# Performance work log

Hardware: AMD Instinct MI355X
Metric: run time of the kernel (lower is better)

The kernel has to match this reference:

```python
import jax, jax.numpy as jnp
import numpy as np
from jax import lax

T, B = 256, 4096
H = 64  # lstm hidden/input size


def setup_inputs() -> dict:
    key = jax.random.key(0)
    ks = jax.random.split(key, 20)
    s = 0.1
    return {
        "x": jax.random.normal(ks[0], (T * B, 9), jnp.float32),
        "done": jax.random.randint(ks[1], (T * B,), 0, 2).astype(jnp.int32),
        "h0": jax.random.normal(ks[2], (1, B, H), jnp.float32),
        "c0": jax.random.normal(ks[3], (1, B, H), jnp.float32),
        # root MLP: Linear(9,32) ReLU Linear(32,64) ReLU (stored [in,out])
        "Wr1": jax.random.normal(ks[4], (9, 32), jnp.float32) * s,
        "br1": jnp.zeros((32,), jnp.float32),
        "Wr2": jax.random.normal(ks[5], (32, H), jnp.float32) * s,
        "br2": jnp.zeros((H,), jnp.float32),
        # LSTM(64,64): gate order i,f,g,o; stored [in, 4H]
        "Wih": jax.random.normal(ks[6], (H, 4 * H), jnp.float32) * s,
        "Whh": jax.random.normal(ks[7], (H, 4 * H), jnp.float32) * s,
        "b_lstm": jnp.zeros((4 * H,), jnp.float32),  # bias_ih + bias_hh (both init 0)
        # critic: Linear(64,16) Tanh Linear(16,8) Tanh Linear(8,1)
        "Wc1": jax.random.normal(ks[8], (H, 16), jnp.float32) * s,
        "bc1": jnp.zeros((16,), jnp.float32),
        "Wc2": jax.random.normal(ks[9], (16, 8), jnp.float32) * s,
        "bc2": jnp.zeros((8,), jnp.float32),
        "Wc3": jax.random.normal(ks[10], (8, 1), jnp.float32) * s,
        "bc3": jnp.zeros((1,), jnp.float32),
    }


def reference(x, done, h0, c0, Wr1, br1, Wr2, br2, Wih, Whh, b_lstm,
              Wc1, bc1, Wc2, bc2, Wc3, bc3):
    b = h0.shape[1]
    # root MLP on all T*B rows at once
    hidden = jax.nn.relu(jax.nn.relu(x @ Wr1 + br1) @ Wr2 + br2)  # [T*B, 64]
    t = hidden.shape[0] // b
    hid = hidden.reshape(t, b, H)
    d = done.reshape(t, b).astype(hidden.dtype)
    # precompute input projection for all timesteps (hoisted out of the scan)
    xp = hid @ Wih + b_lstm  # [T, B, 4H]

    def step(carry, inp):
        h, c = carry
        xpt, dt = inp
        m = (1.0 - dt)[:, None]  # reset state where episode is done
        h = h * m
        c = c * m
        g = xpt + h @ Whh  # [B, 4H]
        gi, gf, gg, go = jnp.split(g, 4, axis=-1)
        c = jax.nn.sigmoid(gf) * c + jax.nn.sigmoid(gi) * jnp.tanh(gg)
        h = jax.nn.sigmoid(go) * jnp.tanh(c)
        return (h, c), h

    (_, _), hs = lax.scan(step, (h0[0], c0[0]), (xp, d))
    new_hidden = hs.reshape(t * b, H)  # flatten like torch.cat + flatten(0,1)
    # critic head (get_value)
    v = jnp.tanh(new_hidden @ Wc1 + bc1)
    v = jnp.tanh(v @ Wc2 + bc2)
    return v @ Wc3 + bc3  # [T*B, 1]
```

## Files before the change

### kernel.cpp

```cpp
#include <hip/hip_runtime.h>
#include <hip/hip_bf16.h>


#define TT 256
#define BB 4096
#define TBROWS (TT * BB)
#define LOG2E 1.44269504088896340736f

typedef short bf16x8 __attribute__((ext_vector_type(8)));
typedef float f32x4 __attribute__((ext_vector_type(4)));

__device__ __forceinline__ unsigned bfbits(float x) {
  unsigned u = __float_as_uint(x);
  return (u + 0x7fffu + ((u >> 16) & 1u)) >> 16;
}
__device__ __forceinline__ unsigned pkbf(float lo, float hi) {
  return bfbits(lo) | (bfbits(hi) << 16);
}
__device__ __forceinline__ unsigned short cvt1bf(float x) {
  unsigned pk;
  asm("v_cvt_pk_bf16_f32 %0, %1, %2" : "=v"(pk) : "v"(x), "v"(x));
  return (unsigned short)pk;
}
__device__ __forceinline__ float rcpf_(float x) { return __builtin_amdgcn_rcpf(x); }
__device__ __forceinline__ float exp2f_(float x) { return __builtin_amdgcn_exp2f(x); }

#define BAR_LDS()                                                   \
  do {                                                              \
    asm volatile("s_waitcnt lgkmcnt(0)" ::: "memory");              \
    __builtin_amdgcn_s_barrier();                                   \
    asm volatile("" ::: "memory");                                  \
  } while (0)

__global__ __launch_bounds__(256) void k1m(const float* __restrict__ x,
                                           const float* __restrict__ Wr1,
                                           const float* __restrict__ br1,
                                           const float* __restrict__ Wr2,
                                           const float* __restrict__ br2,
                                           unsigned short* __restrict__ hb) {
  __shared__ int sBr1[2 * 256];
  __shared__ int sBr2[4 * 256];
  __shared__ float sx[4][208];
  __shared__ int h1s[4][324];

  const int tid = threadIdx.x;
  const int lane = tid & 63, wid = tid >> 6;
  const int g4 = lane >> 4, l15 = lane & 15;

  for (int i = tid; i < 512; i += 256) {
    int nt = i >> 8, rem = i & 255;
    int L = rem >> 2, d = rem & 3;
    int u = nt * 16 + (L & 15);
    int k0 = (L >> 4) * 4 + d;
    float v0 = (k0 < 9) ? Wr1[k0 * 32 + u] : 0.f;
    sBr1[i] = (int)bfbits(v0);
  }
  for (int i = tid; i < 1024; i += 256) {
    int nt = i >> 8, rem = i & 255;
    int L = rem >> 2, d = rem & 3;
    int u = nt * 16 + (L & 15);
    int p = (L >> 4) * 4 + d;
    sBr2[i] = (int)pkbf(Wr2[p * 64 + u], Wr2[(p + 16) * 64 + u]);
  }
  __syncthreads();

  float br1v[2] = {br1[l15], br1[16 + l15]};
  float br2v[4];
#pragma unroll
  for (int nt = 0; nt < 4; ++nt) br2v[nt] = br2[nt * 16 + l15];

  long gw = (long)blockIdx.x * 4 + wid;
  long nw = (long)gridDim.x * 4;
  for (long row0 = gw * 16; row0 < TBROWS; row0 += nw * 16) {
    {
      int j = lane;
      float v = x[row0 * 9 + j];
      int r = (j * 456) >> 12; int cc = j - r * 9;
      sx[wid][r * 12 + cc] = v;
      j = lane + 64;
      v = x[row0 * 9 + j];
      r = (j * 456) >> 12; cc = j - r * 9;
      sx[wid][r * 12 + cc] = v;
      if (lane < 16) {
        j = lane + 128;
        v = x[row0 * 9 + j];
        r = (j * 456) >> 12; cc = j - r * 9;
        sx[wid][r * 12 + cc] = v;
      }
    }
    float4 xq = *(const float4*)&sx[wid][l15 * 12 + g4 * 4];
    union { unsigned u[4]; bf16x8 v; } A1;
#pragma unroll
    for (int d = 0; d < 4; ++d) {
      float v = ((const float*)&xq)[d];
      v = (g4 * 4 + d < 9) ? v : 0.f;
      A1.u[d] = bfbits(v);
    }
    f32x4 c1[2];
#pragma unroll
    for (int nt = 0; nt < 2; ++nt) {
      c1[nt] = (f32x4){br1v[nt], br1v[nt], br1v[nt], br1v[nt]};
      c1[nt] = __builtin_amdgcn_mfma_f32_16x16x32_bf16(
          A1.v, *(const bf16x8*)&sBr1[nt * 256 + lane * 4], c1[nt], 0, 0, 0);
    }
#pragma unroll
    for (int r = 0; r < 4; ++r)
      h1s[wid][(g4 * 4 + r) * 20 + l15] =
          (int)pkbf(fmaxf(c1[0][r], 0.f), fmaxf(c1[1][r], 0.f));
    bf16x8 A2 = *(const bf16x8*)&h1s[wid][l15 * 20 + g4 * 4];
    f32x4 c2[4];
#pragma unroll
    for (int nt = 0; nt < 4; ++nt) {
      c2[nt] = (f32x4){br2v[nt], br2v[nt], br2v[nt], br2v[nt]};
      c2[nt] = __builtin_amdgcn_mfma_f32_16x16x32_bf16(
          A2, *(const bf16x8*)&sBr2[nt * 256 + lane * 4], c2[nt], 0, 0, 0);
    }
#pragma unroll
    for (int nt = 0; nt < 4; ++nt)
#pragma unroll
      for (int r = 0; r < 4; ++r)
        hb[(row0 + g4 * 4 + r) * 64 + nt * 16 + l15] =
            (unsigned short)bfbits(fmaxf(c2[nt][r], 0.f));
  }
}

__global__ __launch_bounds__(320) void k2m(
    const unsigned short* __restrict__ hb, const int* __restrict__ done,
    const float* __restrict__ h0, const float* __restrict__ c0,
    const float* __restrict__ Wih, const float* __restrict__ Whh,
    const float* __restrict__ bl,
    const float* __restrict__ Wc1, const float* __restrict__ bc1,
    const float* __restrict__ Wc2, const float* __restrict__ bc2,
    const float* __restrict__ Wc3, const float* __restrict__ bc3,
    float* __restrict__ out) {
  __shared__ __align__(16) unsigned short hT2[2][16 * 72];
  __shared__ float sv1[16 * 20];
  __shared__ __align__(16) float smask[TT * 16];
  __shared__ int sdn[TT * 16];

  const int tid = threadIdx.x;
  const int lane = tid & 63;
  const int wid = tid >> 6;
  const int g4 = lane >> 4, l15 = lane & 15;
  const int base_b = blockIdx.x * 16;

  for (int i = tid; i < TT * 16; i += 320) {
    int d = done[(long)(i >> 4) * BB + base_b + (i & 15)];
    sdn[i] = d;
    smask[i] = 1.f - (float)d;
  }

  union frag { unsigned u[4]; bf16x8 v; };
  frag Bih[4][2], Bhh[4][2];
  frag Bc1[2];
  float wc2a[16], wc2b[16];
  float c[4];
  f32x4 bias_acc[4];
  float bc1s = 0.f, bc2s0 = 0.f, bc2s1 = 0.f, wc3a = 0.f, wc3b = 0.f, bc3r = 0.f;

  if (wid < 4) {
#pragma unroll
    for (int g = 0; g < 4; ++g) {
      int nt = g * 4 + wid;
      int col = nt * 16 + l15;
      float sc = (g == 2) ? 2.f * LOG2E : LOG2E;
#pragma unroll
      for (int q = 0; q < 2; ++q)
#pragma unroll
        for (int d = 0; d < 4; ++d) {
          int k0 = q * 32 + g4 * 8 + 2 * d;
          Bih[g][q].u[d] = pkbf(Wih[k0 * 256 + col] * sc, Wih[(k0 + 1) * 256 + col] * sc);
          Bhh[g][q].u[d] = pkbf(Whh[k0 * 256 + col] * sc, Whh[(k0 + 1) * 256 + col] * sc);
        }
      float bv = bl[nt * 16 + l15] * sc;
      bias_acc[g] = (f32x4){bv, bv, bv, bv};
    }
#pragma unroll
    for (int r = 0; r < 4; ++r) {
      int row = base_b + g4 * 4 + r;
      float m0 = 1.f - (float)done[row];
      c[r] = c0[row * 64 + wid * 16 + l15] * m0;
      hT2[1][(g4 * 4 + r) * 72 + wid * 16 + l15] =
          (unsigned short)bfbits(h0[row * 64 + wid * 16 + l15]);
    }
  } else {
    float S = 2.f * LOG2E;
#pragma unroll
    for (int q = 0; q < 2; ++q)
#pragma unroll
      for (int d = 0; d < 4; ++d) {
        int k0 = q * 32 + g4 * 8 + 2 * d;
        Bc1[q].u[d] = pkbf(Wc1[k0 * 16 + l15] * S, Wc1[(k0 + 1) * 16 + l15] * S);
      }
#pragma unroll
    for (int k = 0; k < 16; ++k) {
      wc2a[k] = Wc2[k * 8 + g4 * 2] * S;
      wc2b[k] = Wc2[k * 8 + g4 * 2 + 1] * S;
    }
    bc1s = bc1[l15] * S;
    bc2s0 = bc2[g4 * 2] * S;
    bc2s1 = bc2[g4 * 2 + 1] * S;
    wc3a = Wc3[g4 * 2];
    wc3b = Wc3[g4 * 2 + 1];
    bc3r = bc3[0];
  }
  __syncthreads();

  f32x4 accP[4], accQ[4];
  bf16x8 aA0 = {}, aA1 = {}, aB0 = {}, aB1 = {};
  int dnA = 0, dnB = 0;
  if (wid < 4) {
    long rx = ((long)base_b + l15) * 64;
    bf16x8 x00 = *(const bf16x8*)(hb + rx + g4 * 8);
    bf16x8 x01 = *(const bf16x8*)(hb + rx + 32 + g4 * 8);
#pragma unroll
    for (int g = 0; g < 4; ++g) {
      accP[g] = __builtin_amdgcn_mfma_f32_16x16x32_bf16(x00, Bih[g][0].v, bias_acc[g], 0, 0, 0);
      accP[g] = __builtin_amdgcn_mfma_f32_16x16x32_bf16(x01, Bih[g][1].v, accP[g], 0, 0, 0);
    }
    long r1a = ((long)1 * BB + base_b + l15) * 64;
    long r2a = ((long)2 * BB + base_b + l15) * 64;
    aA0 = *(const bf16x8*)(hb + r1a + g4 * 8);
    aA1 = *(const bf16x8*)(hb + r1a + 32 + g4 * 8);
    aB0 = *(const bf16x8*)(hb + r2a + g4 * 8);
    aB1 = *(const bf16x8*)(hb + r2a + 32 + g4 * 8);
    dnA = sdn[0 * 16 + l15];
    dnB = sdn[1 * 16 + l15];
  }

  auto gate_step = [&](int t, f32x4* accW, f32x4* accN, bf16x8& x0, bf16x8& x1, int& dnv) {
    const unsigned short* rb = hT2[(t + 1) & 1];
    unsigned short* wb = hT2[t & 1];
    __builtin_amdgcn_s_setprio(1);
    int4 r0 = *(const int4*)(rb + l15 * 72 + g4 * 8);
    int4 r1 = *(const int4*)(rb + l15 * 72 + 32 + g4 * 8);
    int tm = (t + 1 < TT) ? t + 1 : t;
    float4 mn4 = *(const float4*)&smask[tm * 16 + g4 * 4];
    if (dnv != 0) { r0 = make_int4(0, 0, 0, 0); r1 = make_int4(0, 0, 0, 0); }
    union { int4 i4; bf16x8 v; } ah0, ah1;
    ah0.i4 = r0; ah1.i4 = r1;
    f32x4 acc[4];
#pragma unroll
    for (int g = 0; g < 4; ++g)
      acc[g] = __builtin_amdgcn_mfma_f32_16x16x32_bf16(ah0.v, Bhh[g][0].v, accW[g], 0, 0, 0);
#pragma unroll
    for (int g = 0; g < 4; ++g)
      acc[g] = __builtin_amdgcn_mfma_f32_16x16x32_bf16(ah1.v, Bhh[g][1].v, acc[g], 0, 0, 0);
    if (t + 1 < TT) {
#pragma unroll
      for (int g = 0; g < 4; ++g)
        accN[g] = __builtin_amdgcn_mfma_f32_16x16x32_bf16(x0, Bih[g][0].v, bias_acc[g], 0, 0, 0);
#pragma unroll
      for (int g = 0; g < 4; ++g)
        accN[g] = __builtin_amdgcn_mfma_f32_16x16x32_bf16(x1, Bih[g][1].v, accN[g], 0, 0, 0);
    }
    if (t + 3 < TT) {
      long nb = ((long)(t + 3) * BB + base_b + l15) * 64;
      x0 = *(const bf16x8*)(hb + nb + g4 * 8);
      x1 = *(const bf16x8*)(hb + nb + 32 + g4 * 8);
    }
    if (t + 2 < TT) dnv = sdn[(t + 2) * 16 + l15];
#pragma unroll
    for (int r = 0; r < 4; ++r) {
      float xi = acc[0][r], xf = acc[1][r], xg = acc[2][r], xo = acc[3][r];
      float si = rcpf_(1.f + exp2f_(-xi));
      float sf = rcpf_(1.f + exp2f_(-xf));
      float so = rcpf_(1.f + exp2f_(-xo));
      float tg = fmaf(2.f, rcpf_(1.f + exp2f_(-xg)), -1.f);
      float cc = fmaf(sf, c[r], si * tg);
      float tc = fmaf(2.f, rcpf_(1.f + exp2f_(cc * (-2.f * LOG2E))), -1.f);
      float oh = so * tc;
      c[r] = cc * ((const float*)&mn4)[r];
      wb[(g4 * 4 + r) * 72 + wid * 16 + l15] = cvt1bf(oh);
    }
    __builtin_amdgcn_s_setprio(0);
  };

  auto critic_step = [&](int tprev, const unsigned short* rb) {
    bf16x8 ca0 = *(const bf16x8*)(rb + l15 * 72 + g4 * 8);
    bf16x8 ca1 = *(const bf16x8*)(rb + l15 * 72 + 32 + g4 * 8);
    f32x4 a1 = (f32x4){bc1s, bc1s, bc1s, bc1s};
    a1 = __builtin_amdgcn_mfma_f32_16x16x32_bf16(ca0, Bc1[0].v, a1, 0, 0, 0);
    a1 = __builtin_amdgcn_mfma_f32_16x16x32_bf16(ca1, Bc1[1].v, a1, 0, 0, 0);
#pragma unroll
    for (int r = 0; r < 4; ++r) {
      float v1 = fmaf(2.f, rcpf_(1.f + exp2f_(-a1[r])), -1.f);
      sv1[(g4 * 4 + r) * 20 + l15] = v1;
    }
    float a2a = bc2s0, a2b = bc2s1;
    const float* vrow = &sv1[l15 * 20];
#pragma unroll
    for (int k = 0; k < 16; ++k) {
      float vk = vrow[k];
      a2a = fmaf(vk, wc2a[k], a2a);
      a2b = fmaf(vk, wc2b[k], a2b);
    }
    float v2a = fmaf(2.f, rcpf_(1.f + exp2f_(-a2a)), -1.f);
    float v2b = fmaf(2.f, rcpf_(1.f + exp2f_(-a2b)), -1.f);
    float p = fmaf(v2a, wc3a, v2b * wc3b);
    p += __shfl_xor(p, 16);
    p += __shfl_xor(p, 32);
    if (g4 == 0) out[(long)tprev * BB + base_b + l15] = p + bc3r;
  };

  for (int t2 = 0; t2 < TT; t2 += 2) {
    if (wid < 4) {
      gate_step(t2, accP, accQ, aA0, aA1, dnA);
    } else {
      if (t2 > 0) critic_step(t2 - 1, hT2[(t2 + 1) & 1]);
    }
    BAR_LDS();
    if (wid < 4) {
      gate_step(t2 + 1, accQ, accP, aB0, aB1, dnB);
    } else {
      critic_step(t2, hT2[(t2 + 2) & 1]);
    }
    BAR_LDS();
  }
  if (wid == 4) critic_step(TT - 1, hT2[(TT - 1) & 1]);
}

extern "C" void kernel_launch(void* const* d_in, const int* in_sizes, int n_in,
                              void* d_out, int out_size, void* d_ws, size_t ws_size,
                              hipStream_t stream) {
  const float* x = (const float*)d_in[0];
  const int* done = (const int*)d_in[1];
  const float* h0 = (const float*)d_in[2];
  const float* c0 = (const float*)d_in[3];
  const float* Wr1 = (const float*)d_in[4];
  const float* br1 = (const float*)d_in[5];
  const float* Wr2 = (const float*)d_in[6];
  const float* br2 = (const float*)d_in[7];
  const float* Wih = (const float*)d_in[8];
  const float* Whh = (const float*)d_in[9];
  const float* bl = (const float*)d_in[10];
  const float* Wc1 = (const float*)d_in[11];
  const float* bc1 = (const float*)d_in[12];
  const float* Wc2 = (const float*)d_in[13];
  const float* bc2 = (const float*)d_in[14];
  const float* Wc3 = (const float*)d_in[15];
  const float* bc3 = (const float*)d_in[16];
  float* out = (float*)d_out;

  unsigned short* hb = (unsigned short*)d_ws;

  k1m<<<dim3(1024), dim3(256), 0, stream>>>(x, Wr1, br1, Wr2, br2, hb);
  k2m<<<dim3(256), dim3(320), 0, stream>>>(hb, done, h0, c0, Wih, Whh, bl,
                                           Wc1, bc1, Wc2, bc2, Wc3, bc3, out);
}
```

Measured before the change: 198.1 us.

## Split critic head out of LSTM recurrence into separate grid-wide kernel

Result: slower. 273.6 us (+38.1%).

```diff
diff --git a/kernel.cpp b/kernel.cpp
--- a/kernel.cpp
+++ b/kernel.cpp
@@ -124,17 +124,13 @@
   }
 }
 
-__global__ __launch_bounds__(320) void k2m(
+__global__ __launch_bounds__(256) void k2m4(
     const unsigned short* __restrict__ hb, const int* __restrict__ done,
     const float* __restrict__ h0, const float* __restrict__ c0,
     const float* __restrict__ Wih, const float* __restrict__ Whh,
     const float* __restrict__ bl,
-    const float* __restrict__ Wc1, const float* __restrict__ bc1,
-    const float* __restrict__ Wc2, const float* __restrict__ bc2,
-    const float* __restrict__ Wc3, const float* __restrict__ bc3,
-    float* __restrict__ out) {
+    unsigned short* __restrict__ hs) {
   __shared__ __align__(16) unsigned short hT2[2][16 * 72];
-  __shared__ float sv1[16 * 20];
   __shared__ __align__(16) float smask[TT * 16];
   __shared__ int sdn[TT * 16];
 
@@ -144,7 +140,7 @@
   const int g4 = lane >> 4, l15 = lane & 15;
   const int base_b = blockIdx.x * 16;
 
-  for (int i = tid; i < TT * 16; i += 320) {
+  for (int i = tid; i < TT * 16; i += 256) {
     int d = done[(long)(i >> 4) * BB + base_b + (i & 15)];
     sdn[i] = d;
     smask[i] = 1.f - (float)d;
@@ -152,64 +148,38 @@
 
   union frag { unsigned u[4]; bf16x8 v; };
   frag Bih[4][2], Bhh[4][2];
-  frag Bc1[2];
-  float wc2a[16], wc2b[16];
   float c[4];
   f32x4 bias_acc[4];
-  float bc1s = 0.f, bc2s0 = 0.f, bc2s1 = 0.f, wc3a = 0.f, wc3b = 0.f, bc3r = 0.f;
-
-  if (wid < 4) {
-#pragma unroll
-    for (int g = 0; g < 4; ++g) {
-      int nt = g * 4 + wid;
-      int col = nt * 16 + l15;
-      float sc = (g == 2) ? 2.f * LOG2E : LOG2E;
-#pragma unroll
-      for (int q = 0; q < 2; ++q)
-#pragma unroll
-        for (int d = 0; d < 4; ++d) {
-          int k0 = q * 32 + g4 * 8 + 2 * d;
-          Bih[g][q].u[d] = pkbf(Wih[k0 * 256 + col] * sc, Wih[(k0 + 1) * 256 + col] * sc);
-          Bhh[g][q].u[d] = pkbf(Whh[k0 * 256 + col] * sc, Whh[(k0 + 1) * 256 + col] * sc);
-        }
-      float bv = bl[nt * 16 + l15] * sc;
-      bias_acc[g] = (f32x4){bv, bv, bv, bv};
-    }
-#pragma unroll
-    for (int r = 0; r < 4; ++r) {
-      int row = base_b + g4 * 4 + r;
-      float m0 = 1.f - (float)done[row];
-      c[r] = c0[row * 64 + wid * 16 + l15] * m0;
-      hT2[1][(g4 * 4 + r) * 72 + wid * 16 + l15] =
-          (unsigned short)bfbits(h0[row * 64 + wid * 16 + l15]);
-    }
-  } else {
-    float S = 2.f * LOG2E;
+
+#pragma unroll
+  for (int g = 0; g < 4; ++g) {
+    int nt = g * 4 + wid;
+    int col = nt * 16 + l15;
+    float sc = (g == 2) ? 2.f * LOG2E : LOG2E;
 #pragma unroll
     for (int q = 0; q < 2; ++q)
 #pragma unroll
       for (int d = 0; d < 4; ++d) {
         int k0 = q * 32 + g4 * 8 + 2 * d;
-        Bc1[q].u[d] = pkbf(Wc1[k0 * 16 + l15] * S, Wc1[(k0 + 1) * 16 + l15] * S);
+        Bih[g][q].u[d] = pkbf(Wih[k0 * 256 + col] * sc, Wih[(k0 + 1) * 256 + col] * sc);
+        Bhh[g][q].u[d] = pkbf(Whh[k0 * 256 + col] * sc, Whh[(k0 + 1) * 256 + col] * sc);
       }
-#pragma unroll
-    for (int k = 0; k < 16; ++k) {
-      wc2a[k] = Wc2[k * 8 + g4 * 2] * S;
-      wc2b[k] = Wc2[k * 8 + g4 * 2 + 1] * S;
-    }
-    bc1s = bc1[l15] * S;
-    bc2s0 = bc2[g4 * 2] * S;
-    bc2s1 = bc2[g4 * 2 + 1] * S;
-    wc3a = Wc3[g4 * 2];
-    wc3b = Wc3[g4 * 2 + 1];
-    bc3r = bc3[0];
+    float bv = bl[nt * 16 + l15] * sc;
+    bias_acc[g] = (f32x4){bv, bv, bv, bv};
+  }
+#pragma unroll
+  for (int r = 0; r < 4; ++r) {
+    int row = base_b + g4 * 4 + r;
+    float m0 = 1.f - (float)done[row];
+    c[r] = c0[row * 64 + wid * 16 + l15] * m0;
+    hT2[1][(g4 * 4 + r) * 72 + wid * 16 + l15] =
+        (unsigned short)bfbits(h0[row * 64 + wid * 16 + l15]);
   }
   __syncthreads();
 
   f32x4 accP[4], accQ[4];
-  bf16x8 aA0 = {}, aA1 = {}, aB0 = {}, aB1 = {};
-  int dnA = 0, dnB = 0;
-  if (wid < 4) {
+  bf16x8 xb0, xb1;
+  {
     long rx = ((long)base_b + l15) * 64;
     bf16x8 x00 = *(const bf16x8*)(hb + rx + g4 * 8);
     bf16x8 x01 = *(const bf16x8*)(hb + rx + 32 + g4 * 8);
@@ -219,24 +189,20 @@
       accP[g] = __builtin_amdgcn_mfma_f32_16x16x32_bf16(x01, Bih[g][1].v, accP[g], 0, 0, 0);
     }
     long r1a = ((long)1 * BB + base_b + l15) * 64;
-    long r2a = ((long)2 * BB + base_b + l15) * 64;
-    aA0 = *(const bf16x8*)(hb + r1a + g4 * 8);
-    aA1 = *(const bf16x8*)(hb + r1a + 32 + g4 * 8);
-    aB0 = *(const bf16x8*)(hb + r2a + g4 * 8);
-    aB1 = *(const bf16x8*)(hb + r2a + 32 + g4 * 8);
-    dnA = sdn[0 * 16 + l15];
-    dnB = sdn[1 * 16 + l15];
-  }
-
-  auto gate_step = [&](int t, f32x4* accW, f32x4* accN, bf16x8& x0, bf16x8& x1, int& dnv) {
+    xb0 = *(const bf16x8*)(hb + r1a + g4 * 8);
+    xb1 = *(const bf16x8*)(hb + r1a + 32 + g4 * 8);
+  }
+
+  auto gate_step = [&](int t, f32x4* accW, f32x4* accN) {
     const unsigned short* rb = hT2[(t + 1) & 1];
     unsigned short* wb = hT2[t & 1];
     __builtin_amdgcn_s_setprio(1);
+    int dn = sdn[t * 16 + l15];
     int4 r0 = *(const int4*)(rb + l15 * 72 + g4 * 8);
     int4 r1 = *(const int4*)(rb + l15 * 72 + 32 + g4 * 8);
     int tm = (t + 1 < TT) ? t + 1 : t;
     float4 mn4 = *(const float4*)&smask[tm * 16 + g4 * 4];
-    if (dnv != 0) { r0 = make_int4(0, 0, 0, 0); r1 = make_int4(0, 0, 0, 0); }
+    if (dn != 0) { r0 = make_int4(0, 0, 0, 0); r1 = make_int4(0, 0, 0, 0); }
     union { int4 i4; bf16x8 v; } ah0, ah1;
     ah0.i4 = r0; ah1.i4 = r1;
     f32x4 acc[4];
@@ -249,17 +215,12 @@
     if (t + 1 < TT) {
 #pragma unroll
       for (int g = 0; g < 4; ++g)
-        accN[g] = __builtin_amdgcn_mfma_f32_16x16x32_bf16(x0, Bih[g][0].v, bias_acc[g], 0, 0, 0);
+        accN[g] = __builtin_amdgcn_mfma_f32_16x16x32_bf16(xb0, Bih[g][0].v, bias_acc[g], 0, 0, 0);
 #pragma unroll
       for (int g = 0; g < 4; ++g)
-        accN[g] = __builtin_amdgcn_mfma_f32_16x16x32_bf16(x1, Bih[g][1].v, accN[g], 0, 0, 0);
-    }
-    if (t + 3 < TT) {
-      long nb = ((long)(t + 3) * BB + base_b + l15) * 64;
-      x0 = *(const bf16x8*)(hb + nb + g4 * 8);
-      x1 = *(const bf16x8*)(hb + nb + 32 + g4 * 8);
-    }
-    if (t + 2 < TT) dnv = sdn[(t + 2) * 16 + l15];
+        accN[g] = __builtin_amdgcn_mfma_f32_16x16x32_bf16(xb1, Bih[g][1].v, accN[g], 0, 0, 0);
+    }
+    unsigned short* hsp = hs + ((long)t * BB + base_b + g4 * 4) * 64 + wid * 16 + l15;
 #pragma unroll
     for (int r = 0; r < 4; ++r) {
       float xi = acc[0][r], xf = acc[1][r], xg = acc[2][r], xo = acc[3][r];
@@ -271,24 +232,79 @@
       float tc = fmaf(2.f, rcpf_(1.f + exp2f_(cc * (-2.f * LOG2E))), -1.f);
       float oh = so * tc;
       c[r] = cc * ((const float*)&mn4)[r];
-      wb[(g4 * 4 + r) * 72 + wid * 16 + l15] = cvt1bf(oh);
+      unsigned short ohb = cvt1bf(oh);
+      wb[(g4 * 4 + r) * 72 + wid * 16 + l15] = ohb;
+      hsp[(long)r * 64] = ohb;
+    }
+    if (t + 2 < TT) {
+      long nb = ((long)(t + 2) * BB + base_b + l15) * 64;
+      xb0 = *(const bf16x8*)(hb + nb + g4 * 8);
+      xb1 = *(const bf16x8*)(hb + nb + 32 + g4 * 8);
     }
     __builtin_amdgcn_s_setprio(0);
   };
 
-  auto critic_step = [&](int tprev, const unsigned short* rb) {
-    bf16x8 ca0 = *(const bf16x8*)(rb + l15 * 72 + g4 * 8);
-    bf16x8 ca1 = *(const bf16x8*)(rb + l15 * 72 + 32 + g4 * 8);
+  for (int t2 = 0; t2 < TT; t2 += 2) {
+    gate_step(t2, accP, accQ);
+    BAR_LDS();
+    gate_step(t2 + 1, accQ, accP);
+    BAR_LDS();
+  }
+}
+
+__global__ __launch_bounds__(256) void kcritm(const unsigned short* __restrict__ hs,
+                                              const float* __restrict__ Wc1,
+                                              const float* __restrict__ bc1,
+                                              const float* __restrict__ Wc2,
+                                              const float* __restrict__ bc2,
+                                              const float* __restrict__ Wc3,
+                                              const float* __restrict__ bc3,
+                                              float* __restrict__ out) {
+  __shared__ float sv1[4][16 * 20];
+
+  const int tid = threadIdx.x;
+  const int lane = tid & 63;
+  const int wid = tid >> 6;
+  const int g4 = lane >> 4, l15 = lane & 15;
+
+  union frag { unsigned u[4]; bf16x8 v; };
+  frag Bc1[2];
+  float wc2a[16], wc2b[16];
+  const float S = 2.f * LOG2E;
+#pragma unroll
+  for (int q = 0; q < 2; ++q)
+#pragma unroll
+    for (int d = 0; d < 4; ++d) {
+      int k0 = q * 32 + g4 * 8 + 2 * d;
+      Bc1[q].u[d] = pkbf(Wc1[k0 * 16 + l15] * S, Wc1[(k0 + 1) * 16 + l15] * S);
+    }
+#pragma unroll
+  for (int k = 0; k < 16; ++k) {
+    wc2a[k] = Wc2[k * 8 + g4 * 2] * S;
+    wc2b[k] = Wc2[k * 8 + g4 * 2 + 1] * S;
+  }
+  float bc1s = bc1[l15] * S;
+  float bc2s0 = bc2[g4 * 2] * S;
+  float bc2s1 = bc2[g4 * 2 + 1] * S;
+  float wc3a = Wc3[g4 * 2];
+  float wc3b = Wc3[g4 * 2 + 1];
+  float bc3r = bc3[0];
+
+  long gw = (long)blockIdx.x * 4 + wid;
+  long nw = (long)gridDim.x * 4;
+  for (long row0 = gw * 16; row0 < TBROWS; row0 += nw * 16) {
+    bf16x8 ca0 = *(const bf16x8*)(hs + (row0 + l15) * 64 + g4 * 8);
+    bf16x8 ca1 = *(const bf16x8*)(hs + (row0 + l15) * 64 + 32 + g4 * 8);
     f32x4 a1 = (f32x4){bc1s, bc1s, bc1s, bc1s};
     a1 = __builtin_amdgcn_mfma_f32_16x16x32_bf16(ca0, Bc1[0].v, a1, 0, 0, 0);
     a1 = __builtin_amdgcn_mfma_f32_16x16x32_bf16(ca1, Bc1[1].v, a1, 0, 0, 0);
 #pragma unroll
     for (int r = 0; r < 4; ++r) {
       float v1 = fmaf(2.f, rcpf_(1.f + exp2f_(-a1[r])), -1.f);
-      sv1[(g4 * 4 + r) * 20 + l15] = v1;
+      sv1[wid][(g4 * 4 + r) * 20 + l15] = v1;
     }
     float a2a = bc2s0, a2b = bc2s1;
-    const float* vrow = &sv1[l15 * 20];
+    const float* vrow = &sv1[wid][l15 * 20];
 #pragma unroll
     for (int k = 0; k < 16; ++k) {
       float vk = vrow[k];
@@ -300,24 +316,8 @@
     float p = fmaf(v2a, wc3a, v2b * wc3b);
     p += __shfl_xor(p, 16);
     p += __shfl_xor(p, 32);
-    if (g4 == 0) out[(long)tprev * BB + base_b + l15] = p + bc3r;
-  };
-
-  for (int t2 = 0; t2 < TT; t2 += 2) {
-    if (wid < 4) {
-      gate_step(t2, accP, accQ, aA0, aA1, dnA);
-    } else {
-      if (t2 > 0) critic_step(t2 - 1, hT2[(t2 + 1) & 1]);
-    }
-    BAR_LDS();
-    if (wid < 4) {
-      gate_step(t2 + 1, accQ, accP, aB0, aB1, dnB);
-    } else {
-      critic_step(t2, hT2[(t2 + 2) & 1]);
-    }
-    BAR_LDS();
-  }
-  if (wid == 4) critic_step(TT - 1, hT2[(TT - 1) & 1]);
+    if (g4 == 0) out[row0 + l15] = p + bc3r;
+  }
 }
 
 extern "C" void kernel_launch(void* const* d_in, const int* in_sizes, int n_in,
@@ -343,8 +343,9 @@
   float* out = (float*)d_out;
 
   unsigned short* hb = (unsigned short*)d_ws;
+  unsigned short* hs = hb + (size_t)TBROWS * 64;
 
   k1m<<<dim3(1024), dim3(256), 0, stream>>>(x, Wr1, br1, Wr2, br2, hb);
-  k2m<<<dim3(256), dim3(320), 0, stream>>>(hb, done, h0, c0, Wih, Whh, bl,
-                                           Wc1, bc1, Wc2, bc2, Wc3, bc3, out);
-}
+  k2m4<<<dim3(256), dim3(256), 0, stream>>>(hb, done, h0, c0, Wih, Whh, bl, hs);
+  kcritm<<<dim3(1024), dim3(256), 0, stream>>>(hs, Wc1, bc1, Wc2, bc2, Wc3, bc3, out);
+}
```
